# Optimization experiments

Hardware: AMD Instinct MI355X
Metric: run time of the kernel (lower is better)

The kernel has to match this reference:

```python
import jax, jax.numpy as jnp
import numpy as np

B, S, H = 4, 2048, 1024

def setup_inputs() -> dict:
    key = jax.random.key(0)
    k = jax.random.split(key, 5)
    scale = 1.0 / np.sqrt(H)
    return {
        "hidden": jax.random.normal(k[0], (B, S, H), dtype=jnp.float32),
        "mask": jnp.zeros((B, 1, S, S), dtype=jnp.float32),
        "R": jax.random.normal(k[1], (S, S), dtype=jnp.float32),
        "G_w": jax.random.normal(k[2], (H, H), dtype=jnp.float32) * scale,
        "G_b": jnp.zeros((H,), dtype=jnp.float32),
        "F_w": jax.random.normal(k[3], (H, H), dtype=jnp.float32) * scale,
        "F_b": jnp.zeros((H,), dtype=jnp.float32),
    }

def reference(hidden, mask, R, G_w, G_b, F_w, F_b):
    # scores: [B, S, S] = learned random bias + additive attention mask
    scores = R + mask[:, 0]
    probs = jax.nn.softmax(scores, axis=-1)  # dropout is identity in eval mode
    values = jnp.einsum('bsh,oh->bso', hidden, G_w) + G_b  # G_linear
    out = jnp.einsum('bqk,bkh->bqh', probs, values)
    out = jnp.einsum('bsh,oh->bso', out, F_w) + F_b  # final_linear
    return out
```

## Files before the change

### kernel.cpp

```cpp
#include <hip/hip_runtime.h>
#include <hip/hip_bf16.h>

typedef __bf16 bf16x8 __attribute__((ext_vector_type(8)));
typedef __bf16 bf16x4 __attribute__((ext_vector_type(4)));
typedef float  f32x16 __attribute__((ext_vector_type(16)));

#define GPTR(p) ((__attribute__((address_space(1))) void*)(p))
#define LPTR(p) ((__attribute__((address_space(3))) void*)(p))

__global__ __launch_bounds__(256) void phase_a_kernel(
    const float* __restrict__ hidden, __bf16* __restrict__ h_bf,
    const float* __restrict__ Fw, __bf16* __restrict__ f_bf,
    const float* __restrict__ Gw, __bf16* __restrict__ gt_bf,
    const float* __restrict__ Gb, const float* __restrict__ Fb,
    float* __restrict__ b2, int H) {
    __shared__ float tile[64][65];
    const int blk = blockIdx.x;
    const int t = threadIdx.x;

    if (blk < 4096) {
        long i = ((long)blk * 256 + t) * 8;
        float4 a = *reinterpret_cast<const float4*>(hidden + i);
        float4 c = *reinterpret_cast<const float4*>(hidden + i + 4);
        bf16x8 o;
        o[0] = (__bf16)a.x; o[1] = (__bf16)a.y; o[2] = (__bf16)a.z; o[3] = (__bf16)a.w;
        o[4] = (__bf16)c.x; o[5] = (__bf16)c.y; o[6] = (__bf16)c.z; o[7] = (__bf16)c.w;
        *reinterpret_cast<bf16x8*>(h_bf + i) = o;
    } else if (blk < 4608) {
        long i = ((long)(blk - 4096) * 256 + t) * 8;
        float4 a = *reinterpret_cast<const float4*>(Fw + i);
        float4 c = *reinterpret_cast<const float4*>(Fw + i + 4);
        bf16x8 o;
        o[0] = (__bf16)a.x; o[1] = (__bf16)a.y; o[2] = (__bf16)a.z; o[3] = (__bf16)a.w;
        o[4] = (__bf16)c.x; o[5] = (__bf16)c.y; o[6] = (__bf16)c.z; o[7] = (__bf16)c.w;
        *reinterpret_cast<bf16x8*>(f_bf + i) = o;
    } else if (blk < 4864) {
        const int id = blk - 4608;
        const int bx = (id & 15) * 64;
        const int by = (id >> 4) * 64;
        const int tr = t >> 4;
        const int tc = (t & 15) * 4;
#pragma unroll
        for (int i = 0; i < 4; i++) {
            float4 v = *reinterpret_cast<const float4*>(&Gw[(size_t)(by + tr + i * 16) * H + bx + tc]);
            tile[tr + i * 16][tc + 0] = v.x;
            tile[tr + i * 16][tc + 1] = v.y;
            tile[tr + i * 16][tc + 2] = v.z;
            tile[tr + i * 16][tc + 3] = v.w;
        }
        __syncthreads();
        const int wr = t >> 2;
        const int wc = (t & 3) * 16;
        bf16x8 o0, o1;
#pragma unroll
        for (int j = 0; j < 8; j++) o0[j] = (__bf16)tile[wc + j][wr];
#pragma unroll
        for (int j = 0; j < 8; j++) o1[j] = (__bf16)tile[wc + 8 + j][wr];
        *reinterpret_cast<bf16x8*>(&gt_bf[(size_t)(bx + wr) * H + by + wc]) = o0;
        *reinterpret_cast<bf16x8*>(&gt_bf[(size_t)(bx + wr) * H + by + wc + 8]) = o1;
    } else {
        const int o = blk - 4864;
        float s = 0.f;
        for (int h = t; h < H; h += 256) s += Fw[(size_t)o * H + h] * Gb[h];
#pragma unroll
        for (int off = 32; off > 0; off >>= 1) s += __shfl_xor(s, off);
        __shared__ float ss[4];
        if ((t & 63) == 0) ss[t >> 6] = s;
        __syncthreads();
        if (t == 0) b2[o] = ss[0] + ss[1] + ss[2] + ss[3] + Fb[o];
    }
}

__global__ __launch_bounds__(256) void phase_b_kernel(
    const __bf16* __restrict__ f_bf, const __bf16* __restrict__ gt_bf,
    __bf16* __restrict__ Wm, const float* __restrict__ R,
    const float* __restrict__ mask, __bf16* __restrict__ P, int H, int S) {
    const int blk = blockIdx.x;
    const int t = threadIdx.x;

    if (blk < 256) {
        __shared__ __bf16 As[64 * 64];
        __shared__ __bf16 Bs[64 * 64];
        const int lane = t & 63;
        const int wave = t >> 6;
        const int lane31 = lane & 31;
        const int hi = lane >> 5;
        const int wm = (wave >> 1) * 32;
        const int wn = (wave & 1) * 32;
        const int bm = (blk >> 4) * 64;
        const int bn = (blk & 15) * 64;

        const int rsub = lane >> 3;
        const int csub = lane & 7;
        const int lchunk = csub ^ rsub;
        const __bf16* ga0 = f_bf + (size_t)(bm + wave * 16 + rsub) * H + lchunk * 8;
        const __bf16* gb0 = gt_bf + (size_t)(bn + wave * 16 + rsub) * H + lchunk * 8;

        f32x16 acc = (f32x16)(0.f);
        for (int kt = 0; kt < H; kt += 64) {
            __syncthreads();
#pragma unroll
            for (int c = 0; c < 2; c++)
                __builtin_amdgcn_global_load_lds(GPTR(ga0 + (size_t)(c * 8) * H + kt),
                                                 LPTR(&As[(wave * 16 + c * 8) * 64]), 16, 0, 0);
#pragma unroll
            for (int c = 0; c < 2; c++)
                __builtin_amdgcn_global_load_lds(GPTR(gb0 + (size_t)(c * 8) * H + kt),
                                                 LPTR(&Bs[(wave * 16 + c * 8) * 64]), 16, 0, 0);
            __syncthreads();
#pragma unroll
            for (int s = 0; s < 4; s++) {
                const int ra = wm + lane31;
                const int rb = wn + lane31;
                bf16x8 af = *reinterpret_cast<const bf16x8*>(
                    &As[ra * 64 + (((2 * s + hi) ^ (ra & 7)) << 3)]);
                bf16x8 bfr = *reinterpret_cast<const bf16x8*>(
                    &Bs[rb * 64 + (((2 * s + hi) ^ (rb & 7)) << 3)]);
                acc = __builtin_amdgcn_mfma_f32_32x32x16_bf16(af, bfr, acc, 0, 0, 0);
            }
        }
        const int cm = bm + wm;
        const int cn = bn + wn + lane31;
#pragma unroll
        for (int rq = 0; rq < 4; rq++) {
            const int rbase = rq * 8 + 4 * hi;
#pragma unroll
            for (int rr = 0; rr < 4; rr++)
                Wm[(size_t)(cm + rbase + rr) * H + cn] = (__bf16)acc[rq * 4 + rr];
        }
    } else {
        const int id = blk - 256;
        const int b = id >> 11;
        const int q = id & 2047;
        const int lane = t & 63, wave = t >> 6;
        const float* rrow = R + (size_t)q * S;
        const float* mrow = mask + ((size_t)b * S + q) * (size_t)S;
        __bf16* prow = P + ((size_t)b * S + q) * (size_t)S;

        float v[8];
#pragma unroll
        for (int i = 0; i < 2; i++) {
            float4 r4 = *reinterpret_cast<const float4*>(rrow + t * 8 + i * 4);
            float4 m4 = *reinterpret_cast<const float4*>(mrow + t * 8 + i * 4);
            v[i * 4 + 0] = r4.x + m4.x;
            v[i * 4 + 1] = r4.y + m4.y;
            v[i * 4 + 2] = r4.z + m4.z;
            v[i * 4 + 3] = r4.w + m4.w;
        }
        float mx = v[0];
#pragma unroll
        for (int i = 1; i < 8; i++) mx = fmaxf(mx, v[i]);
#pragma unroll
        for (int off = 32; off > 0; off >>= 1) mx = fmaxf(mx, __shfl_xor(mx, off));
        __shared__ float smax[4], ssum[4];
        if (lane == 0) smax[wave] = mx;
        __syncthreads();
        mx = fmaxf(fmaxf(smax[0], smax[1]), fmaxf(smax[2], smax[3]));
        float sum = 0.f;
#pragma unroll
        for (int i = 0; i < 8; i++) { v[i] = __expf(v[i] - mx); sum += v[i]; }
#pragma unroll
        for (int off = 32; off > 0; off >>= 1) sum += __shfl_xor(sum, off);
        if (lane == 0) ssum[wave] = sum;
        __syncthreads();
        sum = ssum[0] + ssum[1] + ssum[2] + ssum[3];
        const float inv = 1.0f / sum;
        bf16x8 o;
#pragma unroll
        for (int i = 0; i < 8; i++) o[i] = (__bf16)(v[i] * inv);
        *reinterpret_cast<bf16x8*>(prow + t * 8) = o;
    }
}

template <bool TRANSC, bool CFLOAT, bool BIAS, bool SWZ>
__global__ __launch_bounds__(128) void gemm_nt_kernel(
    const __bf16* __restrict__ A, const __bf16* __restrict__ B,
    const float* __restrict__ bias, void* __restrict__ Cv,
    int K, int lda, int ldb, int ldc,
    long strideA, long strideB, long strideC) {
    const int t = threadIdx.x;
    const int lane = t & 63;
    const int wave = t >> 6;
    const int lane31 = lane & 31;
    const int hi = lane >> 5;
    int bm, bn, bz;
    if constexpr (SWZ) {
        const int id = blockIdx.x;
        const int xcd = id & 7;
        const int slot = id >> 3;
        bz = xcd >> 1;
        bm = ((xcd & 1) * 16 + (slot >> 3)) * 64;
        bn = (slot & 7) * 128;
    } else {
        bm = blockIdx.y * 64;
        bn = blockIdx.x * 128;
        bz = blockIdx.z;
    }

    A += (size_t)bz * strideA;
    B += (size_t)bz * strideB;

    __shared__ __bf16 smem[12288];
    __bf16* const As = smem;
    __bf16* const Bs = smem + 4096;

    const int rsub = lane >> 3;
    const int csub = lane & 7;
    const int lchunk = csub ^ rsub;
    const __bf16* ga0 = A + (size_t)(bm + wave * 32 + rsub) * lda + lchunk * 8;
    const __bf16* gb0 = B + (size_t)(bn + wave * 64 + rsub) * ldb + lchunk * 8;

    f32x16 acc[2][2];
#pragma unroll
    for (int i = 0; i < 2; i++)
#pragma unroll
        for (int j = 0; j < 2; j++) acc[i][j] = (f32x16)(0.f);

    for (int kt = 0; kt < K; kt += 64) {
        __syncthreads();
#pragma unroll
        for (int c = 0; c < 4; c++)
            __builtin_amdgcn_global_load_lds(GPTR(ga0 + (size_t)(c * 8) * lda + kt),
                                             LPTR(&As[(wave * 32 + c * 8) * 64]), 16, 0, 0);
#pragma unroll
        for (int c = 0; c < 8; c++)
            __builtin_amdgcn_global_load_lds(GPTR(gb0 + (size_t)(c * 8) * ldb + kt),
                                             LPTR(&Bs[(wave * 64 + c * 8) * 64]), 16, 0, 0);
        __syncthreads();
#pragma unroll
        for (int s = 0; s < 4; s++) {
            bf16x8 af[2], bfr[2];
#pragma unroll
            for (int mi = 0; mi < 2; mi++) {
                const int r = mi * 32 + lane31;
                af[mi] = *reinterpret_cast<const bf16x8*>(
                    &As[r * 64 + (((2 * s + hi) ^ (r & 7)) << 3)]);
            }
#pragma unroll
            for (int ni = 0; ni < 2; ni++) {
                const int r = wave * 64 + ni * 32 + lane31;
                bfr[ni] = *reinterpret_cast<const bf16x8*>(
                    &Bs[r * 64 + (((2 * s + hi) ^ (r & 7)) << 3)]);
            }
#pragma unroll
            for (int mi = 0; mi < 2; mi++)
#pragma unroll
                for (int ni = 0; ni < 2; ni++)
                    acc[mi][ni] = __builtin_amdgcn_mfma_f32_32x32x16_bf16(af[mi], bfr[ni], acc[mi][ni], 0, 0, 0);
        }
    }

    if constexpr (TRANSC) {
        __syncthreads();
        __bf16* sC = smem;
#pragma unroll
        for (int mi = 0; mi < 2; mi++)
#pragma unroll
            for (int ni = 0; ni < 2; ni++)
#pragma unroll
                for (int rq = 0; rq < 4; rq++) {
                    const int n_l = wave * 64 + ni * 32 + lane31;
                    const int m_l = mi * 32 + rq * 8 + 4 * hi;
                    bf16x4 pk;
#pragma unroll
                    for (int rr = 0; rr < 4; rr++) pk[rr] = (__bf16)acc[mi][ni][rq * 4 + rr];
                    *reinterpret_cast<bf16x4*>(&sC[n_l * 72 + m_l]) = pk;
                }
        __syncthreads();
        __bf16* Ct = (__bf16*)Cv + (size_t)bz * strideC;
        const int col = (t & 7) * 8;
#pragma unroll
        for (int p = 0; p < 8; p++) {
            const int row = p * 16 + (t >> 3);
            bf16x8 v = *reinterpret_cast<const bf16x8*>(&sC[row * 72 + col]);
            *reinterpret_cast<bf16x8*>(Ct + (size_t)(bn + row) * ldc + bm + col) = v;
        }
    } else {
        __bf16* Cb = (__bf16*)Cv + (size_t)bz * strideC;
        float* Cf = (float*)Cv + (size_t)bz * strideC;
#pragma unroll
        for (int mi = 0; mi < 2; mi++)
#pragma unroll
            for (int ni = 0; ni < 2; ni++) {
                const int cm = bm + mi * 32;
                const int cn = bn + wave * 64 + ni * 32 + lane31;
                const float bv = BIAS ? bias[cn] : 0.0f;
#pragma unroll
                for (int rq = 0; rq < 4; rq++) {
                    const int rbase = rq * 8 + 4 * hi;
                    if constexpr (CFLOAT) {
#pragma unroll
                        for (int rr = 0; rr < 4; rr++)
                            Cf[(size_t)(cm + rbase + rr) * ldc + cn] = acc[mi][ni][rq * 4 + rr] + bv;
                    } else {
#pragma unroll
                        for (int rr = 0; rr < 4; rr++)
                            Cb[(size_t)(cm + rbase + rr) * ldc + cn] = (__bf16)(acc[mi][ni][rq * 4 + rr] + bv);
                    }
                }
            }
    }
}

extern "C" void kernel_launch(void* const* d_in, const int* in_sizes, int n_in,
                              void* d_out, int out_size, void* d_ws, size_t ws_size,
                              hipStream_t stream) {
    const float* hidden = (const float*)d_in[0];
    const float* mask   = (const float*)d_in[1];
    const float* R      = (const float*)d_in[2];
    const float* G_w    = (const float*)d_in[3];
    const float* G_b    = (const float*)d_in[4];
    const float* F_w    = (const float*)d_in[5];
    const float* F_b    = (const float*)d_in[6];
    float* out = (float*)d_out;

    constexpr int B = 4, S = 2048, H = 1024;
    char* ws = (char*)d_ws;
    __bf16* h_bf  = (__bf16*)(ws);
    __bf16* vt    = (__bf16*)(ws + (16ll << 20));
    __bf16* probs = (__bf16*)(ws + (32ll << 20));
    __bf16* f_bf  = (__bf16*)(ws + (64ll << 20));
    __bf16* gt_bf = (__bf16*)(ws + (66ll << 20));
    __bf16* Wm    = (__bf16*)(ws + (68ll << 20));
    float*  b2    = (float*)(ws + (70ll << 20));

    phase_a_kernel<<<5888, 256, 0, stream>>>(hidden, h_bf, F_w, f_bf, G_w, gt_bf,
                                             G_b, F_b, b2, H);

    phase_b_kernel<<<256 + B * S, 256, 0, stream>>>(f_bf, gt_bf, Wm, R, mask, probs, H, S);

    gemm_nt_kernel<true, false, false, false><<<dim3(H / 128, S / 64, B), 128, 0, stream>>>(
        h_bf, Wm, nullptr, vt, H, H, H,  S,
        (long)S * H, 0, (long)H * S);

    gemm_nt_kernel<false, true, true, true><<<1024, 128, 0, stream>>>(
        probs, vt, b2, out, S, S, S, H,
        (long)S * S, (long)H * S, (long)S * H);
}
```

Before: 237.4 us.

## Reassociate to compute probs·hidden first, then one flattened GEMM with fused weights

The product order changes from probs·(hidden·Wmᵀ) to (probs·hidden)·Wmᵀ. Hidden is now transposed and converted to bf16 inside the middle kernel, alongside the softmax and weight-fusion blocks. The final projection becomes a single flattened 8192×1024×1024 GEMM with its own XCD-aware block mapping. This removes the transposed-store epilogue and the separate hidden conversion, so the prep work spreads across fewer dependent phases. The cost is a bf16 rounding of a different intermediate, which slightly changes numerics.

```diff
diff --git a/kernel.cpp b/kernel.cpp
--- a/kernel.cpp
+++ b/kernel.cpp
@@ -8,8 +8,7 @@
 #define GPTR(p) ((__attribute__((address_space(1))) void*)(p))
 #define LPTR(p) ((__attribute__((address_space(3))) void*)(p))
 
-__global__ __launch_bounds__(256) void phase_a_kernel(
-    const float* __restrict__ hidden, __bf16* __restrict__ h_bf,
+__global__ __launch_bounds__(256) void pre_kernel(
     const float* __restrict__ Fw, __bf16* __restrict__ f_bf,
     const float* __restrict__ Gw, __bf16* __restrict__ gt_bf,
     const float* __restrict__ Gb, const float* __restrict__ Fb,
@@ -18,24 +17,16 @@
     const int blk = blockIdx.x;
     const int t = threadIdx.x;
 
-    if (blk < 4096) {
+    if (blk < 512) {
         long i = ((long)blk * 256 + t) * 8;
-        float4 a = *reinterpret_cast<const float4*>(hidden + i);
-        float4 c = *reinterpret_cast<const float4*>(hidden + i + 4);
-        bf16x8 o;
-        o[0] = (__bf16)a.x; o[1] = (__bf16)a.y; o[2] = (__bf16)a.z; o[3] = (__bf16)a.w;
-        o[4] = (__bf16)c.x; o[5] = (__bf16)c.y; o[6] = (__bf16)c.z; o[7] = (__bf16)c.w;
-        *reinterpret_cast<bf16x8*>(h_bf + i) = o;
-    } else if (blk < 4608) {
-        long i = ((long)(blk - 4096) * 256 + t) * 8;
         float4 a = *reinterpret_cast<const float4*>(Fw + i);
         float4 c = *reinterpret_cast<const float4*>(Fw + i + 4);
         bf16x8 o;
         o[0] = (__bf16)a.x; o[1] = (__bf16)a.y; o[2] = (__bf16)a.z; o[3] = (__bf16)a.w;
         o[4] = (__bf16)c.x; o[5] = (__bf16)c.y; o[6] = (__bf16)c.z; o[7] = (__bf16)c.w;
         *reinterpret_cast<bf16x8*>(f_bf + i) = o;
-    } else if (blk < 4864) {
-        const int id = blk - 4608;
+    } else if (blk < 768) {
+        const int id = blk - 512;
         const int bx = (id & 15) * 64;
         const int by = (id >> 4) * 64;
         const int tr = t >> 4;
@@ -59,7 +50,7 @@
         *reinterpret_cast<bf16x8*>(&gt_bf[(size_t)(bx + wr) * H + by + wc]) = o0;
         *reinterpret_cast<bf16x8*>(&gt_bf[(size_t)(bx + wr) * H + by + wc + 8]) = o1;
     } else {
-        const int o = blk - 4864;
+        const int o = blk - 768;
         float s = 0.f;
         for (int h = t; h < H; h += 256) s += Fw[(size_t)o * H + h] * Gb[h];
 #pragma unroll
@@ -71,10 +62,12 @@
     }
 }
 
-__global__ __launch_bounds__(256) void phase_b_kernel(
+__global__ __launch_bounds__(256) void mid_kernel(
     const __bf16* __restrict__ f_bf, const __bf16* __restrict__ gt_bf,
-    __bf16* __restrict__ Wm, const float* __restrict__ R,
-    const float* __restrict__ mask, __bf16* __restrict__ P, int H, int S) {
+    __bf16* __restrict__ Wm,
+    const float* __restrict__ hidden, __bf16* __restrict__ xt,
+    const float* __restrict__ R, const float* __restrict__ mask,
+    __bf16* __restrict__ P, int H, int S) {
     const int blk = blockIdx.x;
     const int t = threadIdx.x;
 
@@ -128,8 +121,37 @@
             for (int rr = 0; rr < 4; rr++)
                 Wm[(size_t)(cm + rbase + rr) * H + cn] = (__bf16)acc[rq * 4 + rr];
         }
+    } else if (blk < 2304) {
+        __shared__ float tile[64][65];
+        const int id = blk - 256;
+        const int b = id >> 9;
+        const int tid = id & 511;
+        const int by = (tid >> 4) * 64;
+        const int bx = (tid & 15) * 64;
+        const float* x = hidden + (size_t)b * S * H;
+        __bf16* y = xt + (size_t)b * H * S;
+        const int tr = t >> 4;
+        const int tc = (t & 15) * 4;
+#pragma unroll
+        for (int i = 0; i < 4; i++) {
+            float4 v = *reinterpret_cast<const float4*>(&x[(size_t)(by + tr + i * 16) * H + bx + tc]);
+            tile[tr + i * 16][tc + 0] = v.x;
+            tile[tr + i * 16][tc + 1] = v.y;
+            tile[tr + i * 16][tc + 2] = v.z;
+            tile[tr + i * 16][tc + 3] = v.w;
+        }
+        __syncthreads();
+        const int wr = t >> 2;
+        const int wc = (t & 3) * 16;
+        bf16x8 o0, o1;
+#pragma unroll
+        for (int j = 0; j < 8; j++) o0[j] = (__bf16)tile[wc + j][wr];
+#pragma unroll
+        for (int j = 0; j < 8; j++) o1[j] = (__bf16)tile[wc + 8 + j][wr];
+        *reinterpret_cast<bf16x8*>(&y[(size_t)(bx + wr) * S + by + wc]) = o0;
+        *reinterpret_cast<bf16x8*>(&y[(size_t)(bx + wr) * S + by + wc + 8]) = o1;
     } else {
-        const int id = blk - 256;
+        const int id = blk - 2304;
         const int b = id >> 11;
         const int q = id & 2047;
         const int lane = t & 63, wave = t >> 6;
@@ -172,7 +194,7 @@
     }
 }
 
-template <bool TRANSC, bool CFLOAT, bool BIAS, bool SWZ>
+template <bool CFLOAT, bool BIAS, int SWZMODE>
 __global__ __launch_bounds__(128) void gemm_nt_kernel(
     const __bf16* __restrict__ A, const __bf16* __restrict__ B,
     const float* __restrict__ bias, void* __restrict__ Cv,
@@ -184,13 +206,20 @@
     const int lane31 = lane & 31;
     const int hi = lane >> 5;
     int bm, bn, bz;
-    if constexpr (SWZ) {
+    if constexpr (SWZMODE == 1) {
         const int id = blockIdx.x;
         const int xcd = id & 7;
         const int slot = id >> 3;
         bz = xcd >> 1;
         bm = ((xcd & 1) * 16 + (slot >> 3)) * 64;
         bn = (slot & 7) * 128;
+    } else if constexpr (SWZMODE == 2) {
+        const int id = blockIdx.x;
+        const int xcd = id & 7;
+        const int slot = id >> 3;
+        bz = 0;
+        bm = (xcd * 16 + (slot >> 3)) * 64;
+        bn = (slot & 7) * 128;
     } else {
         bm = blockIdx.y * 64;
         bn = blockIdx.x * 128;
@@ -250,56 +279,29 @@
         }
     }
 
-    if constexpr (TRANSC) {
-        __syncthreads();
-        __bf16* sC = smem;
-#pragma unroll
-        for (int mi = 0; mi < 2; mi++)
-#pragma unroll
-            for (int ni = 0; ni < 2; ni++)
-#pragma unroll
-                for (int rq = 0; rq < 4; rq++) {
-                    const int n_l = wave * 64 + ni * 32 + lane31;
-                    const int m_l = mi * 32 + rq * 8 + 4 * hi;
-                    bf16x4 pk;
-#pragma unroll
-                    for (int rr = 0; rr < 4; rr++) pk[rr] = (__bf16)acc[mi][ni][rq * 4 + rr];
-                    *reinterpret_cast<bf16x4*>(&sC[n_l * 72 + m_l]) = pk;
-                }
-        __syncthreads();
-        __bf16* Ct = (__bf16*)Cv + (size_t)bz * strideC;
-        const int col = (t & 7) * 8;
-#pragma unroll
-        for (int p = 0; p < 8; p++) {
-            const int row = p * 16 + (t >> 3);
-            bf16x8 v = *reinterpret_cast<const bf16x8*>(&sC[row * 72 + col]);
-            *reinterpret_cast<bf16x8*>(Ct + (size_t)(bn + row) * ldc + bm + col) = v;
-        }
-    } else {
-        __bf16* Cb = (__bf16*)Cv + (size_t)bz * strideC;
-        float* Cf = (float*)Cv + (size_t)bz * strideC;
-#pragma unroll
-        for (int mi = 0; mi < 2; mi++)
-#pragma unroll
-            for (int ni = 0; ni < 2; ni++) {
-                const int cm = bm + mi * 32;
-                const int cn = bn + wave * 64 + ni * 32 + lane31;
-                const float bv = BIAS ? bias[cn] : 0.0f;
-#pragma unroll
-                for (int rq = 0; rq < 4; rq++) {
-                    const int rbase = rq * 8 + 4 * hi;
-                    if constexpr (CFLOAT) {
-#pragma unroll
-                        for (int rr = 0; rr < 4; rr++)
-                            Cf[(size_t)(cm + rbase + rr) * ldc + cn] = acc[mi][ni][rq * 4 + rr] + bv;
-                    } else {
-#pragma unroll
-                        for (int rr = 0; rr < 4; rr++)
-                            Cb[(size_t)(cm + rbase + rr) * ldc + cn] = (__bf16)(acc[mi][ni][rq * 4 + rr] + bv);
-                    }
+    __bf16* Cb = (__bf16*)Cv + (size_t)bz * strideC;
+    float* Cf = (float*)Cv + (size_t)bz * strideC;
+#pragma unroll
+    for (int mi = 0; mi < 2; mi++)
+#pragma unroll
+        for (int ni = 0; ni < 2; ni++) {
+            const int cm = bm + mi * 32;
+            const int cn = bn + wave * 64 + ni * 32 + lane31;
+            const float bv = BIAS ? bias[cn] : 0.0f;
+#pragma unroll
+            for (int rq = 0; rq < 4; rq++) {
+                const int rbase = rq * 8 + 4 * hi;
+                if constexpr (CFLOAT) {
+#pragma unroll
+                    for (int rr = 0; rr < 4; rr++)
+                        Cf[(size_t)(cm + rbase + rr) * ldc + cn] = acc[mi][ni][rq * 4 + rr] + bv;
+                } else {
+#pragma unroll
+                    for (int rr = 0; rr < 4; rr++)
+                        Cb[(size_t)(cm + rbase + rr) * ldc + cn] = (__bf16)(acc[mi][ni][rq * 4 + rr] + bv);
                 }
             }
-    }
+        }
 }
 
 extern "C" void kernel_launch(void* const* d_in, const int* in_sizes, int n_in,
@@ -316,24 +318,23 @@
 
     constexpr int B = 4, S = 2048, H = 1024;
     char* ws = (char*)d_ws;
-    __bf16* h_bf  = (__bf16*)(ws);
-    __bf16* vt    = (__bf16*)(ws + (16ll << 20));
+    __bf16* xt    = (__bf16*)(ws);
+    __bf16* t1    = (__bf16*)(ws + (16ll << 20));
     __bf16* probs = (__bf16*)(ws + (32ll << 20));
     __bf16* f_bf  = (__bf16*)(ws + (64ll << 20));
     __bf16* gt_bf = (__bf16*)(ws + (66ll << 20));
     __bf16* Wm    = (__bf16*)(ws + (68ll << 20));
     float*  b2    = (float*)(ws + (70ll << 20));
 
-    phase_a_kernel<<<5888, 256, 0, stream>>>(hidden, h_bf, F_w, f_bf, G_w, gt_bf,
-                                             G_b, F_b, b2, H);
-
-    phase_b_kernel<<<256 + B * S, 256, 0, stream>>>(f_bf, gt_bf, Wm, R, mask, probs, H, S);
-
-    gemm_nt_kernel<true, false, false, false><<<dim3(H / 128, S / 64, B), 128, 0, stream>>>(
-        h_bf, Wm, nullptr, vt, H, H, H,  S,
-        (long)S * H, 0, (long)H * S);
-
-    gemm_nt_kernel<false, true, true, true><<<1024, 128, 0, stream>>>(
-        probs, vt, b2, out, S, S, S, H,
+    pre_kernel<<<1792, 256, 0, stream>>>(F_w, f_bf, G_w, gt_bf, G_b, F_b, b2, H);
+
+    mid_kernel<<<10496, 256, 0, stream>>>(f_bf, gt_bf, Wm, hidden, xt,
+                                          R, mask, probs, H, S);
+
+    gemm_nt_kernel<false, false, 1><<<1024, 128, 0, stream>>>(
+        probs, xt, nullptr, t1, S, S, S, H,
         (long)S * S, (long)H * S, (long)S * H);
+
+    gemm_nt_kernel<true, true, 2><<<1024, 128, 0, stream>>>(
+        t1, Wm, b2, out, H, H, H, H, 0, 0, 0);
 }
```

After: 236.2 us. No clear change (-0.5%).
